# Kernel tuning notes

Measured on AMD Instinct MI355X. Metric: run time of the kernel, lower is better.

The kernel has to match this reference:

```python
import jax, jax.numpy as jnp
import numpy as np

B, V, J = 1024, 6890, 24
P_FEAT = (J - 1) * 9  # 207 pose-blendshape features
SMPL_PARENTS = [-1, 0, 0, 0, 1, 2, 3, 4, 5, 6, 7, 8, 9, 9, 9, 12, 13, 14, 16, 17, 18, 19, 20, 21]


def setup_inputs() -> dict:
    key = jax.random.key(0)
    ks = jax.random.split(key, 7)
    return {
        "betas": jax.random.normal(ks[0], (B, 10), jnp.float32),
        "full_pose": jax.random.normal(ks[1], (B, 72), jnp.float32) * 0.3,
        "v_template": jax.random.normal(ks[2], (1, V, 3), jnp.float32),
        "shapedirs": jax.random.normal(ks[3], (V, 3, 10), jnp.float32) * 0.01,
        "posedirs": jax.random.normal(ks[4], (P_FEAT, V * 3), jnp.float32) * 0.01,
        "J_regressor": jax.nn.softmax(jax.random.normal(ks[5], (J, V), jnp.float32), axis=-1),
        "lbs_weights": jax.nn.softmax(jax.random.normal(ks[6], (V, J), jnp.float32) * 4.0, axis=-1),
        "parents": jnp.array(SMPL_PARENTS, dtype=jnp.int32),
    }


def batch_rodrigues(rot_vecs):
    # rot_vecs: [..., 3] axis-angle -> [..., 3, 3] rotation matrices
    angle = jnp.linalg.norm(rot_vecs + 1e-8, axis=-1, keepdims=True)  # [...,1]
    axis = rot_vecs / angle
    s = jnp.sin(angle)[..., None]
    c = jnp.cos(angle)[..., None]
    kx, ky, kz = axis[..., 0], axis[..., 1], axis[..., 2]
    zeros = jnp.zeros_like(kx)
    K = jnp.stack([zeros, -kz, ky, kz, zeros, -kx, -ky, kx, zeros], axis=-1)
    K = K.reshape(rot_vecs.shape[:-1] + (3, 3))
    eye = jnp.eye(3, dtype=rot_vecs.dtype)
    return eye + s * K + (1.0 - c) * (K @ K)


def reference(betas, full_pose, v_template, shapedirs, posedirs, J_regressor, lbs_weights, parents):
    p = [int(x) for x in np.asarray(jax.device_get(parents))]  # static kinematic tree
    b = betas.shape[0]

    # 1) shape blendshapes: minimal shape
    v_shaped = v_template + jnp.einsum("bl,vkl->bvk", betas, shapedirs)  # [B,V,3]

    # 2) rest joints
    J_rest = jnp.einsum("jv,bvk->bjk", J_regressor, v_shaped)  # [B,J,3]

    # 3) pose rotations + pose blendshapes
    rot_mats = batch_rodrigues(full_pose.reshape(b, J, 3))  # [B,J,3,3]
    eye = jnp.eye(3, dtype=rot_mats.dtype)
    pose_feature = (rot_mats[:, 1:] - eye).reshape(b, P_FEAT)  # [B,207]
    v_posed = v_shaped + (pose_feature @ posedirs).reshape(b, V, 3)

    # 4) kinematic chain (sequential composition over fixed 24 joints)
    rel_joints = J_rest.at[:, 1:].add(-J_rest[:, np.array(p[1:])])  # [B,J,3]
    Tm = jnp.zeros((b, J, 4, 4), dtype=rot_mats.dtype)
    Tm = Tm.at[:, :, :3, :3].set(rot_mats)
    Tm = Tm.at[:, :, :3, 3].set(rel_joints)
    Tm = Tm.at[:, :, 3, 3].set(1.0)
    chain = [Tm[:, 0]]
    for i in range(1, J):
        chain.append(chain[p[i]] @ Tm[:, i])
    transforms = jnp.stack(chain, axis=1)  # [B,J,4,4]

    J_posed = transforms[:, :, :3, 3]  # [B,J,3]

    # relative bone transforms: subtract rotated rest joints from translation
    RJ = jnp.einsum("bjmn,bjn->bjm", transforms[:, :, :3, :3], J_rest)
    A = transforms.at[:, :, :3, 3].add(-RJ)  # [B,J,4,4]

    # 5) linear blend skinning: per-vertex weighted transform then apply
    T = jnp.einsum("vj,bjmn->bvmn", lbs_weights, A)  # [B,V,4,4]
    verts = jnp.einsum("bvmn,bvn->bvm", T[:, :, :3, :3], v_posed) + T[:, :, :3, 3]

    return verts, J_posed, J_rest, A, v_shaped
```

## Files before the change

### kernel.cpp

```cpp
#include <hip/hip_runtime.h>
#include <hip/hip_bf16.h>

#define BDIM 1024
#define VDIM 6890
#define NJ   24
#define NCOL (VDIM*3)
#define KPAD 224
#define NPAD 20736
#define NB   8
#define VPAD 6912
#define MB   16

#define OUT_VERTS   0
#define OUT_JPOSED  21166080
#define OUT_JREST   21239808
#define OUT_A       21313536
#define OUT_VSHAPED 21706752

#define SCRF_PDT    0
#define SCRF_PF     2322432
#define SCRF_JTJS   2437120

#define WSB_PDT   0u
#define WSB_PF    9289728u
#define WSB_JTJS  9748480u
#define WSB_WHI   9752064u
#define WSB_WLO   10194432u
#define WSB_AHI   10636800u
#define WSB_ALO   11685376u
#define WS_NEED   12733952u

typedef __hip_bfloat16 bf16;
typedef unsigned short ushort_t;
typedef __attribute__((ext_vector_type(8))) short  short8;
typedef __attribute__((ext_vector_type(4))) float  float4v;

__device__ __forceinline__ bf16  tob(float x) { return __float2bfloat16(x); }

__device__ __forceinline__ ushort_t bf16_rne(float x) {
    unsigned u = __builtin_bit_cast(unsigned, x);
    unsigned r = (u + 0x7FFFu + ((u >> 16) & 1u)) >> 16;
    return (ushort_t)r;
}
__device__ __forceinline__ float bf16_to_f(ushort_t h) {
    unsigned u = ((unsigned)h) << 16;
    return __builtin_bit_cast(float, u);
}

__global__ __launch_bounds__(256) void k_prep2(const float* __restrict__ jreg,
        const float* __restrict__ vt, const float* __restrict__ sd,
        const float* __restrict__ lbs, const float* __restrict__ pd,
        float* __restrict__ jtjs, ushort_t* __restrict__ whi,
        ushort_t* __restrict__ wlo, bf16* __restrict__ pdt) {
    __shared__ float red[4][33];
    __shared__ bf16 tile[32][65];
    int bid = blockIdx.x;
    int t = threadIdx.x;
    if (bid < 24) {
        int j = bid;
        float acc[33];
#pragma unroll
        for (int i = 0; i < 33; i++) acc[i] = 0.f;
        for (int v = t; v < VDIM; v += 256) {
            float r = jreg[j*VDIM + v];
#pragma unroll
            for (int m = 0; m < 3; m++) {
                acc[m] += r * vt[v*3+m];
#pragma unroll
                for (int l = 0; l < 10; l++)
                    acc[3 + m*10 + l] += r * sd[(v*3+m)*10 + l];
            }
        }
        int lane = t & 63, wid = t >> 6;
#pragma unroll
        for (int i = 0; i < 33; i++) {
            float x = acc[i];
            for (int off = 32; off > 0; off >>= 1) x += __shfl_down(x, off);
            if (lane == 0) red[wid][i] = x;
        }
        __syncthreads();
        if (t < 33)
            jtjs[j*33 + t] = red[0][t] + red[1][t] + red[2][t] + red[3][t];
        return;
    }
    if (bid < 888) {
        if (!whi) return;
        int idx = (bid - 24)*256 + t;
        int v = idx >> 5, j = idx & 31;
        float x = (v < VDIM && j < 24) ? lbs[v*24 + j] : 0.f;
        ushort_t h = bf16_rne(x);
        whi[idx] = h;
        wlo[idx] = bf16_rne(x - bf16_to_f(h));
        return;
    }
    int r = bid - 888;
    int nt = (r % 324) * 64;
    int kt = (r / 324) * 32;
    for (int i = t; i < 32*64; i += 256) {
        int kk = i >> 6, nn = i & 63;
        int k = kt + kk, n = nt + nn;
        float v = 0.f;
        if (k < 207 && n < NCOL) v = pd[k*NCOL + n];
        tile[kk][nn] = tob(v);
    }
    __syncthreads();
    {
        int oct = t >> 6, nn = t & 63;
        short8 o;
#pragma unroll
        for (int q = 0; q < 8; q++)
            o[q] = (short)*reinterpret_cast<const ushort_t*>(&tile[oct*8 + q][nn]);
        *reinterpret_cast<short8*>((ushort_t*)pdt + (nt + nn)*KPAD + kt + oct*8) = o;
    }
}

__global__ __launch_bounds__(64) void k_pose(const float* __restrict__ betas,
        const float* __restrict__ pose, const int* __restrict__ parents,
        const float* __restrict__ jtjs, float* __restrict__ out,
        bf16* __restrict__ wspf, ushort_t* __restrict__ ahi,
        ushort_t* __restrict__ alo) {
    int b = blockIdx.x, t = threadIdx.x;
    __shared__ float R[24][9];
    __shared__ float jrest[24][3];
    __shared__ float rel[24][3];
    __shared__ float ch[24][12];
    __shared__ int par[24];
    if (t < 24) {
        par[t] = parents[t];
        float rx = pose[b*72 + t*3 + 0];
        float ry = pose[b*72 + t*3 + 1];
        float rz = pose[b*72 + t*3 + 2];
        float ax = rx + 1e-8f, ay = ry + 1e-8f, az = rz + 1e-8f;
        float angle = sqrtf(ax*ax + ay*ay + az*az);
        float inv = 1.0f / angle;
        float kx = rx*inv, ky = ry*inv, kz = rz*inv;
        float s = sinf(angle), c = cosf(angle);
        float t1 = 1.0f - c;
        float q = kx*kx + ky*ky + kz*kz;
        R[t][0] = 1.f + t1*(kx*kx - q);
        R[t][1] = -s*kz + t1*kx*ky;
        R[t][2] =  s*ky + t1*kx*kz;
        R[t][3] =  s*kz + t1*kx*ky;
        R[t][4] = 1.f + t1*(ky*ky - q);
        R[t][5] = -s*kx + t1*ky*kz;
        R[t][6] = -s*ky + t1*kx*kz;
        R[t][7] =  s*kx + t1*ky*kz;
        R[t][8] = 1.f + t1*(kz*kz - q);
    }
    __syncthreads();
    for (int i = t; i < KPAD; i += 64) {
        float pf = 0.f;
        if (i < 207) {
            int j = i/9 + 1, e = i - (j-1)*9;
            pf = R[j][e] - ((e == 0 || e == 4 || e == 8) ? 1.f : 0.f);
        }
        wspf[b*KPAD + i] = tob(pf);
    }
    for (int i = t; i < 72; i += 64) {
        int j = i/3, k = i - j*3;
        const float* JJ = &jtjs[j*33];
        float s = JJ[k];
#pragma unroll
        for (int l = 0; l < 10; l++) s += JJ[3 + k*10 + l] * betas[b*10 + l];
        jrest[j][k] = s;
        out[OUT_JREST + b*72 + i] = s;
    }
    __syncthreads();
    for (int i = t; i < 72; i += 64) {
        int j = i/3, k = i - j*3;
        rel[j][k] = jrest[j][k] - (j > 0 ? jrest[par[j]][k] : 0.f);
    }
    __syncthreads();
    if (t < 12) {
        int m = t >> 2, n = t & 3;
        ch[0][t] = (n < 3) ? R[0][m*3+n] : rel[0][m];
    }
    __syncthreads();
    for (int i = 1; i < 24; i++) {
        float val = 0.f;
        if (t < 12) {
            int m = t >> 2, n = t & 3;
            int p = par[i];
            if (n < 3)
                val = ch[p][m*4+0]*R[i][n] + ch[p][m*4+1]*R[i][3+n] + ch[p][m*4+2]*R[i][6+n];
            else
                val = ch[p][m*4+0]*rel[i][0] + ch[p][m*4+1]*rel[i][1]
                    + ch[p][m*4+2]*rel[i][2] + ch[p][m*4+3];
        }
        if (t < 12) ch[i][t] = val;
        __syncthreads();
    }
    for (int i = t; i < 72; i += 64) {
        int j = i/3, k = i - j*3;
        out[OUT_JPOSED + b*72 + i] = ch[j][k*4+3];
    }
    for (int i = t; i < 384; i += 64) {
        int j = i >> 4, e = i & 15, m = e >> 2, n = e & 3;
        float v;
        if (m < 3) {
            if (n < 3) v = ch[j][m*4+n];
            else v = ch[j][m*4+3] - (ch[j][m*4+0]*jrest[j][0] + ch[j][m*4+1]*jrest[j][1]
                                   + ch[j][m*4+2]*jrest[j][2]);
        } else v = (n == 3) ? 1.f : 0.f;
        out[OUT_A + b*384 + i] = v;
    }
    if (ahi) {
        for (int i = t; i < 512; i += 64) {
            int e = i >> 5, j = i & 31;
            float v = 0.f;
            if (j < 24 && e < 12) {
                int m = e >> 2, n = e & 3;
                if (n < 3) v = ch[j][m*4+n];
                else v = ch[j][m*4+3] - (ch[j][m*4+0]*jrest[j][0] + ch[j][m*4+1]*jrest[j][1]
                                       + ch[j][m*4+2]*jrest[j][2]);
            }
            ushort_t h = bf16_rne(v);
            ahi[b*512 + i] = h;
            alo[b*512 + i] = bf16_rne(v - bf16_to_f(h));
        }
    }
}

__global__ __launch_bounds__(256, 8) void k_gemmlbs(const bf16* __restrict__ wspf,
        const bf16* __restrict__ wspdt, const float* __restrict__ betas,
        const float* __restrict__ sd, const float* __restrict__ vt,
        const ushort_t* __restrict__ whi, const ushort_t* __restrict__ wlo,
        const ushort_t* __restrict__ ahi, const ushort_t* __restrict__ alo,
        float* __restrict__ out) {
    __shared__ float dtile[MB][260];
    const ushort_t* pf  = (const ushort_t*)wspf;
    const ushort_t* pdt = (const ushort_t*)wspdt;
    int tid  = threadIdx.x;
    int lane = tid & 63, wave = tid >> 6;
    int l15 = lane & 15, quad = lane >> 4;
    int f   = blockIdx.x;
    int xcd = f & 7, ii = f >> 3;
    int vtile = ii >> 3;
    int bg    = (ii & 7) | (xcd << 3);
    int m0 = bg * MB;
    int v0 = vtile * 64;
    int cb = wave * 48;
    int colb = v0*3 + cb;
    int wv = __builtin_amdgcn_readfirstlane(wave);

    {
        float4v acc[3] = {};
        for (int c = 0; c < 7; c++) {
            short8 a = *reinterpret_cast<const short8*>(pf + (m0 + l15)*KPAD + c*32 + quad*8);
            short8 bb[3];
#pragma unroll
            for (int nf = 0; nf < 3; nf++)
                bb[nf] = *reinterpret_cast<const short8*>(pdt + (colb + nf*16 + l15)*KPAD + c*32 + quad*8);
#pragma unroll
            for (int nf = 0; nf < 3; nf++)
                acc[nf] = __builtin_amdgcn_mfma_f32_16x16x32_bf16(a, bb[nf], acc[nf], 0, 0, 0);
        }
#pragma unroll
        for (int nf = 0; nf < 3; nf++) {
            int c0 = cb + nf*16 + l15;
            int vv = c0 / 3, rr = c0 - vv*3;
            int ad = vv*4 + rr;
#pragma unroll
            for (int r = 0; r < 4; r++)
                dtile[quad*4 + r][ad] = acc[nf][r];
        }
    }
    __syncthreads();

    int v = v0 + lane;
    float* vsh = out + OUT_VSHAPED;
    if (v < VDIM) {
        float vtv[3];
#pragma unroll
        for (int m = 0; m < 3; m++) vtv[m] = vt[v*3 + m];
        float sdv[30];
#pragma unroll
        for (int i = 0; i < 30; i++) sdv[i] = sd[v*30 + i];
#pragma unroll 2
        for (int bb2 = 0; bb2 < 4; bb2++) {
            int b  = m0 + wv*4 + bb2;
            int bl = wv*4 + bb2;
            float vs[3];
#pragma unroll
            for (int m = 0; m < 3; m++) {
                float s = vtv[m];
#pragma unroll
                for (int l = 0; l < 10; l++) s += betas[b*10 + l] * sdv[m*10 + l];
                vs[m] = s;
            }
            float4v* slot = reinterpret_cast<float4v*>(&dtile[bl][lane*4]);
            float4v d = *slot;
            float4v vp;
            vp[0] = vs[0] + d[0]; vp[1] = vs[1] + d[1];
            vp[2] = vs[2] + d[2]; vp[3] = 0.f;
            *slot = vp;
            int base = b*NCOL + v*3;
#pragma unroll
            for (int n = 0; n < 3; n++) vsh[base + n] = vs[n];
        }
    }

    short8 bhi[4], blo[4];
#pragma unroll
    for (int nf = 0; nf < 4; nf++) {
        int vv = v0 + nf*16 + l15;
        bhi[nf] = *reinterpret_cast<const short8*>(whi + vv*32 + quad*8);
        blo[nf] = *reinterpret_cast<const short8*>(wlo + vv*32 + quad*8);
    }
    const ushort_t* ah = ahi + (size_t)(m0 + wv*4)*512 + l15*32 + quad*8;
    const ushort_t* al = alo + (size_t)(m0 + wv*4)*512 + l15*32 + quad*8;
#pragma unroll 1
    for (int bb2 = 0; bb2 < 4; bb2++) {
        int bl = wv*4 + bb2;
        short8 a_hi = *reinterpret_cast<const short8*>(ah + (size_t)bb2*512);
        short8 a_lo = *reinterpret_cast<const short8*>(al + (size_t)bb2*512);
#pragma unroll
        for (int nf = 0; nf < 4; nf++) {
            float4v acc = {};
            acc = __builtin_amdgcn_mfma_f32_16x16x32_bf16(a_hi, bhi[nf], acc, 0, 0, 0);
            acc = __builtin_amdgcn_mfma_f32_16x16x32_bf16(a_lo, bhi[nf], acc, 0, 0, 0);
            acc = __builtin_amdgcn_mfma_f32_16x16x32_bf16(a_hi, blo[nf], acc, 0, 0, 0);
            int vl = nf*16 + l15;
            float4v vp = *reinterpret_cast<const float4v*>(&dtile[bl][vl*4]);
            if (quad < 3) {
                float o = acc[3] + acc[0]*vp[0] + acc[1]*vp[1] + acc[2]*vp[2];
                dtile[bl][vl*4 + quad] = o;
            }
        }
    }

    if (v < VDIM) {
#pragma unroll
        for (int bb2 = 0; bb2 < 4; bb2++) {
            int b  = m0 + wv*4 + bb2;
            int bl = wv*4 + bb2;
            float4v o = *reinterpret_cast<const float4v*>(&dtile[bl][lane*4]);
            int base = b*NCOL + v*3;
            out[base + 0] = o[0];
            out[base + 1] = o[1];
            out[base + 2] = o[2];
        }
    }
}

__global__ __launch_bounds__(256) void k_posegemm(const bf16* __restrict__ wspf,
        const bf16* __restrict__ wspdt, float* __restrict__ dout) {
    const ushort_t* pf  = (const ushort_t*)wspf;
    const ushort_t* pdt = (const ushort_t*)wspdt;
    int lane = threadIdx.x & 63;
    int wave = threadIdx.x >> 6;
    int l15 = lane & 15, quad = lane >> 4;
    int m0 = blockIdx.y * 32;
    int n0 = blockIdx.x * 256 + wave * 64;
    float4v acc[2][4] = {};
    for (int c = 0; c < 7; c++) {
        short8 a[2], bb[4];
#pragma unroll
        for (int mf = 0; mf < 2; mf++)
            a[mf] = *reinterpret_cast<const short8*>(pf + (m0 + mf*16 + l15)*KPAD + c*32 + quad*8);
#pragma unroll
        for (int nf = 0; nf < 4; nf++)
            bb[nf] = *reinterpret_cast<const short8*>(pdt + (n0 + nf*16 + l15)*KPAD + c*32 + quad*8);
#pragma unroll
        for (int mf = 0; mf < 2; mf++)
#pragma unroll
            for (int nf = 0; nf < 4; nf++)
                acc[mf][nf] = __builtin_amdgcn_mfma_f32_16x16x32_bf16(a[mf], bb[nf], acc[mf][nf], 0, 0, 0);
    }
#pragma unroll
    for (int mf = 0; mf < 2; mf++)
#pragma unroll
        for (int nf = 0; nf < 4; nf++) {
            int col = n0 + nf*16 + l15;
            if (col < NCOL) {
#pragma unroll
                for (int r = 0; r < 4; r++) {
                    int row = m0 + mf*16 + quad*4 + r;
                    dout[row*NCOL + col] = acc[mf][nf][r];
                }
            }
        }
}

__global__ __launch_bounds__(256) void k_lbs(const float* __restrict__ betas,
        const float* __restrict__ sd, const float* __restrict__ vt,
        const float* __restrict__ lbs, const float* __restrict__ Amat,
        float* __restrict__ out) {
    int tid = threadIdx.x;
    int v = blockIdx.x*256 + tid;
    if (v >= VDIM) return;
    int b0 = blockIdx.y * NB;
    float w[24];
    {
        const float4v* W4 = reinterpret_cast<const float4v*>(lbs + v*24);
#pragma unroll
        for (int q = 0; q < 6; q++) {
            float4v x = W4[q];
#pragma unroll
            for (int e = 0; e < 4; e++) w[q*4+e] = x[e];
        }
    }
    float vtv[3];
#pragma unroll
    for (int m = 0; m < 3; m++) vtv[m] = vt[v*3 + m];
    float sdv[30];
#pragma unroll
    for (int i = 0; i < 30; i++) sdv[i] = sd[v*30 + i];
    float* vsh = out + OUT_VSHAPED;
#pragma unroll 1
    for (int bb = 0; bb < NB; bb++) {
        int b = b0 + bb;
        const float* __restrict__ Ab = Amat + (size_t)b*384;
        float T[12];
#pragma unroll
        for (int e = 0; e < 12; e++) T[e] = 0.f;
#pragma unroll
        for (int j = 0; j < 24; j++) {
#pragma unroll
            for (int e = 0; e < 12; e++)
                T[e] = fmaf(w[j], Ab[j*16 + e], T[e]);
        }
        float vs[3];
#pragma unroll
        for (int m = 0; m < 3; m++) {
            float s = vtv[m];
#pragma unroll
            for (int l = 0; l < 10; l++) s += betas[b*10 + l] * sdv[m*10 + l];
            vs[m] = s;
        }
        int base = b*NCOL + v*3;
        float vp0 = vs[0] + vsh[base + 0];
        float vp1 = vs[1] + vsh[base + 1];
        float vp2 = vs[2] + vsh[base + 2];
#pragma unroll
        for (int m = 0; m < 3; m++) {
            float o = T[m*4+3] + T[m*4]*vp0 + T[m*4+1]*vp1 + T[m*4+2]*vp2;
            out[base + m] = o;
            vsh[base + m] = vs[m];
        }
    }
}

extern "C" void kernel_launch(void* const* d_in, const int* in_sizes, int n_in,
                              void* d_out, int out_size, void* d_ws, size_t ws_size,
                              hipStream_t stream) {
    const float *betas = nullptr, *pose = nullptr, *vt = nullptr, *sd = nullptr,
                *pd = nullptr, *jreg = nullptr, *lbs = nullptr;
    const int* parents = nullptr;
    for (int i = 0; i < n_in; i++) {
        switch (in_sizes[i]) {
            case 10240:   betas = (const float*)d_in[i]; break;
            case 73728:   pose  = (const float*)d_in[i]; break;
            case 20670:   vt    = (const float*)d_in[i]; break;
            case 206700:  sd    = (const float*)d_in[i]; break;
            case 4278690: pd    = (const float*)d_in[i]; break;
            case 24:      parents = (const int*)d_in[i]; break;
            case 165360:
                if (!jreg) jreg = (const float*)d_in[i];
                else       lbs  = (const float*)d_in[i];
                break;
            default: break;
        }
    }
    float* out = (float*)d_out;
    if (d_ws && ws_size >= (size_t)WS_NEED) {
        bf16*     ws_pdt  = (bf16*)((char*)d_ws + WSB_PDT);
        bf16*     ws_pf   = (bf16*)((char*)d_ws + WSB_PF);
        float*    ws_jtjs = (float*)((char*)d_ws + WSB_JTJS);
        ushort_t* ws_whi  = (ushort_t*)((char*)d_ws + WSB_WHI);
        ushort_t* ws_wlo  = (ushort_t*)((char*)d_ws + WSB_WLO);
        ushort_t* ws_ahi  = (ushort_t*)((char*)d_ws + WSB_AHI);
        ushort_t* ws_alo  = (ushort_t*)((char*)d_ws + WSB_ALO);
        k_prep2<<<3156, 256, 0, stream>>>(jreg, vt, sd, lbs, pd, ws_jtjs,
                                          ws_whi, ws_wlo, ws_pdt);
        k_pose<<<BDIM, 64, 0, stream>>>(betas, pose, parents, ws_jtjs, out, ws_pf,
                                        ws_ahi, ws_alo);
        k_gemmlbs<<<108*64, 256, 0, stream>>>(ws_pf, ws_pdt, betas, sd, vt,
                                              ws_whi, ws_wlo, ws_ahi, ws_alo, out);
    } else {
        bf16*  ws_pdt  = (bf16*)(out + SCRF_PDT);
        bf16*  ws_pf   = (bf16*)(out + SCRF_PF);
        float* ws_jtjs = out + SCRF_JTJS;
        k_prep2<<<3156, 256, 0, stream>>>(jreg, vt, sd, lbs, pd, ws_jtjs,
                                          nullptr, nullptr, ws_pdt);
        k_pose<<<BDIM, 64, 0, stream>>>(betas, pose, parents, ws_jtjs, out, ws_pf,
                                        nullptr, nullptr);
        k_posegemm<<<dim3(81, 32), 256, 0, stream>>>(ws_pf, ws_pdt, out + OUT_VSHAPED);
        k_lbs<<<dim3(27, BDIM/NB), 256, 0, stream>>>(betas, sd, vt, lbs, out + OUT_A, out);
    }
}
```

Baseline: 317.7 us.

## Double batch rows per LBS block and pack four poses per block

```diff
diff --git a/kernel.cpp b/kernel.cpp
--- a/kernel.cpp
+++ b/kernel.cpp
@@ -9,7 +9,7 @@
 #define NPAD 20736
 #define NB   8
 #define VPAD 6912
-#define MB   16
+#define MB   32
 
 #define OUT_VERTS   0
 #define OUT_JPOSED  21166080
@@ -114,19 +114,20 @@
     }
 }
 
-__global__ __launch_bounds__(64) void k_pose(const float* __restrict__ betas,
+__global__ __launch_bounds__(256) void k_pose(const float* __restrict__ betas,
         const float* __restrict__ pose, const int* __restrict__ parents,
         const float* __restrict__ jtjs, float* __restrict__ out,
         bf16* __restrict__ wspf, ushort_t* __restrict__ ahi,
         ushort_t* __restrict__ alo) {
-    int b = blockIdx.x, t = threadIdx.x;
-    __shared__ float R[24][9];
-    __shared__ float jrest[24][3];
-    __shared__ float rel[24][3];
-    __shared__ float ch[24][12];
-    __shared__ int par[24];
+    int wave = threadIdx.x >> 6, t = threadIdx.x & 63;
+    int b = blockIdx.x*4 + wave;
+    __shared__ float R[4][24][9];
+    __shared__ float jrest[4][24][3];
+    __shared__ float rel[4][24][3];
+    __shared__ float ch[4][24][12];
+    __shared__ int par[4][24];
     if (t < 24) {
-        par[t] = parents[t];
+        par[wave][t] = parents[t];
         float rx = pose[b*72 + t*3 + 0];
         float ry = pose[b*72 + t*3 + 1];
         float rz = pose[b*72 + t*3 + 2];
@@ -137,22 +138,21 @@
         float s = sinf(angle), c = cosf(angle);
         float t1 = 1.0f - c;
         float q = kx*kx + ky*ky + kz*kz;
-        R[t][0] = 1.f + t1*(kx*kx - q);
-        R[t][1] = -s*kz + t1*kx*ky;
-        R[t][2] =  s*ky + t1*kx*kz;
-        R[t][3] =  s*kz + t1*kx*ky;
-        R[t][4] = 1.f + t1*(ky*ky - q);
-        R[t][5] = -s*kx + t1*ky*kz;
-        R[t][6] = -s*ky + t1*kx*kz;
-        R[t][7] =  s*kx + t1*ky*kz;
-        R[t][8] = 1.f + t1*(kz*kz - q);
-    }
-    __syncthreads();
+        R[wave][t][0] = 1.f + t1*(kx*kx - q);
+        R[wave][t][1] = -s*kz + t1*kx*ky;
+        R[wave][t][2] =  s*ky + t1*kx*kz;
+        R[wave][t][3] =  s*kz + t1*kx*ky;
+        R[wave][t][4] = 1.f + t1*(ky*ky - q);
+        R[wave][t][5] = -s*kx + t1*ky*kz;
+        R[wave][t][6] = -s*ky + t1*kx*kz;
+        R[wave][t][7] =  s*kx + t1*ky*kz;
+        R[wave][t][8] = 1.f + t1*(kz*kz - q);
+    }
     for (int i = t; i < KPAD; i += 64) {
         float pf = 0.f;
         if (i < 207) {
             int j = i/9 + 1, e = i - (j-1)*9;
-            pf = R[j][e] - ((e == 0 || e == 4 || e == 8) ? 1.f : 0.f);
+            pf = R[wave][j][e] - ((e == 0 || e == 4 || e == 8) ? 1.f : 0.f);
         }
         wspf[b*KPAD + i] = tob(pf);
     }
@@ -162,45 +162,43 @@
         float s = JJ[k];
 #pragma unroll
         for (int l = 0; l < 10; l++) s += JJ[3 + k*10 + l] * betas[b*10 + l];
-        jrest[j][k] = s;
+        jrest[wave][j][k] = s;
         out[OUT_JREST + b*72 + i] = s;
     }
-    __syncthreads();
     for (int i = t; i < 72; i += 64) {
         int j = i/3, k = i - j*3;
-        rel[j][k] = jrest[j][k] - (j > 0 ? jrest[par[j]][k] : 0.f);
-    }
-    __syncthreads();
+        rel[wave][j][k] = jrest[wave][j][k] - (j > 0 ? jrest[wave][par[wave][j]][k] : 0.f);
+    }
     if (t < 12) {
         int m = t >> 2, n = t & 3;
-        ch[0][t] = (n < 3) ? R[0][m*3+n] : rel[0][m];
-    }
-    __syncthreads();
+        ch[wave][0][t] = (n < 3) ? R[wave][0][m*3+n] : rel[wave][0][m];
+    }
     for (int i = 1; i < 24; i++) {
-        float val = 0.f;
         if (t < 12) {
             int m = t >> 2, n = t & 3;
-            int p = par[i];
+            int p = par[wave][i];
+            float val;
             if (n < 3)
-                val = ch[p][m*4+0]*R[i][n] + ch[p][m*4+1]*R[i][3+n] + ch[p][m*4+2]*R[i][6+n];
+                val = ch[wave][p][m*4+0]*R[wave][i][n] + ch[wave][p][m*4+1]*R[wave][i][3+n]
+                    + ch[wave][p][m*4+2]*R[wave][i][6+n];
             else
-                val = ch[p][m*4+0]*rel[i][0] + ch[p][m*4+1]*rel[i][1]
-                    + ch[p][m*4+2]*rel[i][2] + ch[p][m*4+3];
-        }
-        if (t < 12) ch[i][t] = val;
-        __syncthreads();
+                val = ch[wave][p][m*4+0]*rel[wave][i][0] + ch[wave][p][m*4+1]*rel[wave][i][1]
+                    + ch[wave][p][m*4+2]*rel[wave][i][2] + ch[wave][p][m*4+3];
+            ch[wave][i][t] = val;
+        }
     }
     for (int i = t; i < 72; i += 64) {
         int j = i/3, k = i - j*3;
-        out[OUT_JPOSED + b*72 + i] = ch[j][k*4+3];
+        out[OUT_JPOSED + b*72 + i] = ch[wave][j][k*4+3];
     }
     for (int i = t; i < 384; i += 64) {
         int j = i >> 4, e = i & 15, m = e >> 2, n = e & 3;
         float v;
         if (m < 3) {
-            if (n < 3) v = ch[j][m*4+n];
-            else v = ch[j][m*4+3] - (ch[j][m*4+0]*jrest[j][0] + ch[j][m*4+1]*jrest[j][1]
-                                   + ch[j][m*4+2]*jrest[j][2]);
+            if (n < 3) v = ch[wave][j][m*4+n];
+            else v = ch[wave][j][m*4+3] - (ch[wave][j][m*4+0]*jrest[wave][j][0]
+                   + ch[wave][j][m*4+1]*jrest[wave][j][1]
+                   + ch[wave][j][m*4+2]*jrest[wave][j][2]);
         } else v = (n == 3) ? 1.f : 0.f;
         out[OUT_A + b*384 + i] = v;
     }
@@ -210,9 +208,10 @@
             float v = 0.f;
             if (j < 24 && e < 12) {
                 int m = e >> 2, n = e & 3;
-                if (n < 3) v = ch[j][m*4+n];
-                else v = ch[j][m*4+3] - (ch[j][m*4+0]*jrest[j][0] + ch[j][m*4+1]*jrest[j][1]
-                                       + ch[j][m*4+2]*jrest[j][2]);
+                if (n < 3) v = ch[wave][j][m*4+n];
+                else v = ch[wave][j][m*4+3] - (ch[wave][j][m*4+0]*jrest[wave][j][0]
+                       + ch[wave][j][m*4+1]*jrest[wave][j][1]
+                       + ch[wave][j][m*4+2]*jrest[wave][j][2]);
             }
             ushort_t h = bf16_rne(v);
             ahi[b*512 + i] = h;
@@ -221,7 +220,7 @@
     }
 }
 
-__global__ __launch_bounds__(256, 8) void k_gemmlbs(const bf16* __restrict__ wspf,
+__global__ __launch_bounds__(256, 4) void k_gemmlbs(const bf16* __restrict__ wspf,
         const bf16* __restrict__ wspdt, const float* __restrict__ betas,
         const float* __restrict__ sd, const float* __restrict__ vt,
         const ushort_t* __restrict__ whi, const ushort_t* __restrict__ wlo,
@@ -235,8 +234,8 @@
     int l15 = lane & 15, quad = lane >> 4;
     int f   = blockIdx.x;
     int xcd = f & 7, ii = f >> 3;
-    int vtile = ii >> 3;
-    int bg    = (ii & 7) | (xcd << 3);
+    int vtile = ii >> 2;
+    int bg    = (ii & 3) | (xcd << 2);
     int m0 = bg * MB;
     int v0 = vtile * 64;
     int cb = wave * 48;
@@ -244,16 +243,20 @@
     int wv = __builtin_amdgcn_readfirstlane(wave);
 
     {
-        float4v acc[3] = {};
+        float4v acc[2][3] = {};
         for (int c = 0; c < 7; c++) {
-            short8 a = *reinterpret_cast<const short8*>(pf + (m0 + l15)*KPAD + c*32 + quad*8);
-            short8 bb[3];
+            short8 a[2], bb[3];
+#pragma unroll
+            for (int mf = 0; mf < 2; mf++)
+                a[mf] = *reinterpret_cast<const short8*>(pf + (m0 + mf*16 + l15)*KPAD + c*32 + quad*8);
 #pragma unroll
             for (int nf = 0; nf < 3; nf++)
                 bb[nf] = *reinterpret_cast<const short8*>(pdt + (colb + nf*16 + l15)*KPAD + c*32 + quad*8);
 #pragma unroll
-            for (int nf = 0; nf < 3; nf++)
-                acc[nf] = __builtin_amdgcn_mfma_f32_16x16x32_bf16(a, bb[nf], acc[nf], 0, 0, 0);
+            for (int mf = 0; mf < 2; mf++)
+#pragma unroll
+                for (int nf = 0; nf < 3; nf++)
+                    acc[mf][nf] = __builtin_amdgcn_mfma_f32_16x16x32_bf16(a[mf], bb[nf], acc[mf][nf], 0, 0, 0);
         }
 #pragma unroll
         for (int nf = 0; nf < 3; nf++) {
@@ -261,8 +264,10 @@
             int vv = c0 / 3, rr = c0 - vv*3;
             int ad = vv*4 + rr;
 #pragma unroll
-            for (int r = 0; r < 4; r++)
-                dtile[quad*4 + r][ad] = acc[nf][r];
+            for (int mf = 0; mf < 2; mf++)
+#pragma unroll
+                for (int r = 0; r < 4; r++)
+                    dtile[mf*16 + quad*4 + r][ad] = acc[mf][nf][r];
         }
     }
     __syncthreads();
@@ -277,9 +282,9 @@
 #pragma unroll
         for (int i = 0; i < 30; i++) sdv[i] = sd[v*30 + i];
 #pragma unroll 2
-        for (int bb2 = 0; bb2 < 4; bb2++) {
-            int b  = m0 + wv*4 + bb2;
-            int bl = wv*4 + bb2;
+        for (int bb2 = 0; bb2 < 8; bb2++) {
+            int b  = m0 + wv*8 + bb2;
+            int bl = wv*8 + bb2;
             float vs[3];
 #pragma unroll
             for (int m = 0; m < 3; m++) {
@@ -307,11 +312,11 @@
         bhi[nf] = *reinterpret_cast<const short8*>(whi + vv*32 + quad*8);
         blo[nf] = *reinterpret_cast<const short8*>(wlo + vv*32 + quad*8);
     }
-    const ushort_t* ah = ahi + (size_t)(m0 + wv*4)*512 + l15*32 + quad*8;
-    const ushort_t* al = alo + (size_t)(m0 + wv*4)*512 + l15*32 + quad*8;
+    const ushort_t* ah = ahi + (size_t)(m0 + wv*8)*512 + l15*32 + quad*8;
+    const ushort_t* al = alo + (size_t)(m0 + wv*8)*512 + l15*32 + quad*8;
 #pragma unroll 1
-    for (int bb2 = 0; bb2 < 4; bb2++) {
-        int bl = wv*4 + bb2;
+    for (int bb2 = 0; bb2 < 8; bb2++) {
+        int bl = wv*8 + bb2;
         short8 a_hi = *reinterpret_cast<const short8*>(ah + (size_t)bb2*512);
         short8 a_lo = *reinterpret_cast<const short8*>(al + (size_t)bb2*512);
 #pragma unroll
@@ -331,9 +336,9 @@
 
     if (v < VDIM) {
 #pragma unroll
-        for (int bb2 = 0; bb2 < 4; bb2++) {
-            int b  = m0 + wv*4 + bb2;
-            int bl = wv*4 + bb2;
+        for (int bb2 = 0; bb2 < 8; bb2++) {
+            int b  = m0 + wv*8 + bb2;
+            int bl = wv*8 + bb2;
             float4v o = *reinterpret_cast<const float4v*>(&dtile[bl][lane*4]);
             int base = b*NCOL + v*3;
             out[base + 0] = o[0];
@@ -473,9 +478,9 @@
         ushort_t* ws_alo  = (ushort_t*)((char*)d_ws + WSB_ALO);
         k_prep2<<<3156, 256, 0, stream>>>(jreg, vt, sd, lbs, pd, ws_jtjs,
                                           ws_whi, ws_wlo, ws_pdt);
-        k_pose<<<BDIM, 64, 0, stream>>>(betas, pose, parents, ws_jtjs, out, ws_pf,
-                                        ws_ahi, ws_alo);
-        k_gemmlbs<<<108*64, 256, 0, stream>>>(ws_pf, ws_pdt, betas, sd, vt,
+        k_pose<<<BDIM/4, 256, 0, stream>>>(betas, pose, parents, ws_jtjs, out, ws_pf,
+                                           ws_ahi, ws_alo);
+        k_gemmlbs<<<108*32, 256, 0, stream>>>(ws_pf, ws_pdt, betas, sd, vt,
                                               ws_whi, ws_wlo, ws_ahi, ws_alo, out);
     } else {
         bf16*  ws_pdt  = (bf16*)(out + SCRF_PDT);
@@ -483,8 +488,8 @@
         float* ws_jtjs = out + SCRF_JTJS;
         k_prep2<<<3156, 256, 0, stream>>>(jreg, vt, sd, lbs, pd, ws_jtjs,
                                           nullptr, nullptr, ws_pdt);
-        k_pose<<<BDIM, 64, 0, stream>>>(betas, pose, parents, ws_jtjs, out, ws_pf,
-                                        nullptr, nullptr);
+        k_pose<<<BDIM/4, 256, 0, stream>>>(betas, pose, parents, ws_jtjs, out, ws_pf,
+                                           nullptr, nullptr);
         k_posegemm<<<dim3(81, 32), 256, 0, stream>>>(ws_pf, ws_pdt, out + OUT_VSHAPED);
         k_lbs<<<dim3(27, BDIM/NB), 256, 0, stream>>>(betas, sd, vt, lbs, out + OUT_A, out);
     }
```

New measurement: 282.5 us. 11.1% less time.
